# Optimization experiments

Hardware: AMD Instinct MI355X
Metric: run time of the kernel (lower is better)

The kernel has to match this reference:

```python
import jax, jax.numpy as jnp
import numpy as np

NUM_BLOCKS = 8
SPARSITY = 0.01
HARD_FRAC = 1.0
LN_EPS = 1e-5


def layer_norm(x, w, b):
    mu = jnp.mean(x, axis=-1, keepdims=True)
    var = jnp.mean(jnp.square(x - mu), axis=-1, keepdims=True)
    return (x - mu) * jax.lax.rsqrt(var + LN_EPS) * w + b


def softshrink(v, lam):
    return jnp.sign(v) * jnp.maximum(jnp.abs(v) - lam, 0.0)


def afno2d(x, w1, b1, w2, b2):
    # x: [B,H,W,C] float32
    bias = x
    B, H, W, C = x.shape
    nb = NUM_BLOCKS
    bs = C // nb
    xf = jnp.fft.rfft2(x, axes=(1, 2), norm='ortho')  # [B,H,W//2+1,C] complex
    Wf = W // 2 + 1
    xf = xf.reshape(B, H, Wf, nb, bs)
    total_modes = H // 2 + 1
    kept = int(total_modes * HARD_FRAC)
    lo = total_modes - kept
    hi = min(H, total_modes + kept)
    xs = xf[:, lo:hi, :kept]  # [B,hs,kept,nb,bs]
    xr, xi = xs.real, xs.imag
    o1r = jax.nn.relu(jnp.einsum('bhwki,kio->bhwko', xr, w1[0])
                      - jnp.einsum('bhwki,kio->bhwko', xi, w1[1]) + b1[0])
    o1i = jax.nn.relu(jnp.einsum('bhwki,kio->bhwko', xi, w1[0])
                      + jnp.einsum('bhwki,kio->bhwko', xr, w1[1]) + b1[1])
    o2r = (jnp.einsum('bhwko,koi->bhwki', o1r, w2[0])
           - jnp.einsum('bhwko,koi->bhwki', o1i, w2[1]) + b2[0])
    o2i = (jnp.einsum('bhwko,koi->bhwki', o1i, w2[0])
           + jnp.einsum('bhwko,koi->bhwki', o1r, w2[1]) + b2[1])
    o2r = softshrink(o2r, SPARSITY)
    o2i = softshrink(o2i, SPARSITY)
    oc = o2r + 1j * o2i
    full = jnp.zeros((B, H, Wf, nb, bs), dtype=oc.dtype)
    full = full.at[:, lo:hi, :kept].set(oc)
    full = full.reshape(B, H, Wf, C)
    out = jnp.fft.irfft2(full, s=(H, W), axes=(1, 2), norm='ortho')
    return out + bias


def setup_inputs() -> dict:
    key = jax.random.key(0)
    ks = jax.random.split(key, 12)
    B, H, W, C = 2, 90, 180, 768
    nb = NUM_BLOCKS
    bs = C // nb
    hidden = 4 * C
    scale = 0.02
    return {
        'x': jax.random.normal(ks[0], (B, H, W, C), jnp.float32),
        'norm1_w': jnp.ones((C,), jnp.float32),
        'norm1_b': jnp.zeros((C,), jnp.float32),
        'w1': scale * jax.random.normal(ks[1], (2, nb, bs, bs), jnp.float32),
        'b1': scale * jax.random.normal(ks[2], (2, nb, bs), jnp.float32),
        'w2': scale * jax.random.normal(ks[3], (2, nb, bs, bs), jnp.float32),
        'b2': scale * jax.random.normal(ks[4], (2, nb, bs), jnp.float32),
        'norm2_w': jnp.ones((C,), jnp.float32),
        'norm2_b': jnp.zeros((C,), jnp.float32),
        'fc1_w': jax.random.normal(ks[5], (C, hidden), jnp.float32) * (1.0 / np.sqrt(C)),
        'fc1_b': jnp.zeros((hidden,), jnp.float32),
        'fc2_w': jax.random.normal(ks[6], (hidden, C), jnp.float32) * (1.0 / np.sqrt(hidden)),
        'fc2_b': jnp.zeros((C,), jnp.float32),
    }


def reference(x, norm1_w, norm1_b, w1, b1, w2, b2, norm2_w, norm2_b,
              fc1_w, fc1_b, fc2_w, fc2_b):
    residual = x
    h = layer_norm(x, norm1_w, norm1_b)
    h = afno2d(h, w1, b1, w2, b2)
    # double_skip=True
    h = h + residual
    residual = h
    h = layer_norm(h, norm2_w, norm2_b)
    h = jax.nn.gelu(h @ fc1_w + fc1_b, approximate=False)
    h = h @ fc2_w + fc2_b
    return h + residual
```

## Files before the change

### kernel.cpp

```cpp
#include <hip/hip_runtime.h>
#include <hip/hip_bf16.h>

#define B_    2
#define H_    90
#define W_    180
#define C_    768
#define WFK   46
#define NBK   8
#define BSK   96
#define HID   3072
#define NTOK  (B_*H_*W_)
#define MPAD  32512
#define NPOS  (B_*H_*WFK)
#define LAM   0.01f

typedef __attribute__((ext_vector_type(8))) short short8;
typedef __attribute__((ext_vector_type(4))) float f32x4;

__device__ __forceinline__ float bf2f(short u) {
    union { unsigned int i; float f; } z;
    z.i = ((unsigned int)(unsigned short)u) << 16;
    return z.f;
}

__device__ __forceinline__ void gload_lds16(const void* g, void* l) {
    __builtin_amdgcn_global_load_lds((const __attribute__((address_space(1))) void*)g,
                                     (__attribute__((address_space(3))) void*)l, 16, 0, 0);
}

__device__ __forceinline__ float gelu_f(float v) {
    float u = v * (0.7978845608028654f + 0.03567740813636141f * v * v);
    float au = fabsf(u);
    float e = __expf(2.f * au);
    float t = 1.f - 2.f / (e + 1.f);
    t = copysignf(t, u);
    return 0.5f * v * (1.f + t);
}

__global__ __launch_bounds__(256) void init_tables_kernel(__hip_bfloat16* Tw, __hip_bfloat16* Twf,
                                                          __hip_bfloat16* Thf, __hip_bfloat16* Thi) {
    int i = blockIdx.x * 256 + threadIdx.x;
    const float S = 0.00785674201318386f;
    if (i < 192 * 96) {
        int w = i / 96, k = i % 96;
        int j = k >> 1, odd = k & 1;
        float val = 0.f;
        if (w < W_ && j < WFK) {
            float th = (float)((w * j) % W_) * (float)(6.283185307179586476925286766559 / 180.0);
            if (odd) val = (j == 0) ? 0.f : -2.f * S * sinf(th);
            else     val = (j == 0) ? S : 2.f * S * cosf(th);
        }
        Tw[i] = __float2bfloat16(val);
    }
    if (i < 96 * 192) {
        int r = i / 192, w = i % 192;
        int wf = r >> 1, odd = r & 1;
        float val = 0.f;
        if (w < W_ && wf < WFK) {
            float th = (float)((w * wf) % W_) * (float)(6.283185307179586476925286766559 / 180.0);
            val = odd ? -S * sinf(th) : S * cosf(th);
        }
        Twf[i] = __float2bfloat16(val);
    }
    if (i < 192 * 192) {
        int r = i / 192, j = i % 192;
        float vf = 0.f, vi = 0.f;
        if (r < 180 && j < 180) {
            int k = r >> 1, ro = r & 1, h = j >> 1, jo = j & 1;
            float th = (float)((k * h) % H_) * (float)(6.283185307179586476925286766559 / 90.0);
            float c = cosf(th), s = sinf(th);
            vf = ro ? (jo ? c : -s) : (jo ? s : c);
            vi = ro ? (jo ? c : s) : (jo ? -s : c);
        }
        Thf[i] = __float2bfloat16(vf);
        Thi[i] = __float2bfloat16(vi);
    }
}

__global__ __launch_bounds__(256) void wprep_kernel(
        const float* __restrict__ w1, const float* __restrict__ b1,
        const float* __restrict__ w2, const float* __restrict__ b2,
        __hip_bfloat16* __restrict__ wbig, float* __restrict__ bbig)
{
    int idx = blockIdx.x * 256 + threadIdx.x;
    if (idx < 2 * NBK * 192 * 192) {
        int k = idx % 192;
        int o = (idx / 192) % 192;
        int nb = (idx / (192 * 192)) % NBK;
        int L = idx / (192 * 192 * NBK);
        const float* w = L ? w2 : w1;
        const float* wr = w + (size_t)nb * BSK * BSK;
        const float* wi = w + (size_t)(NBK + nb) * BSK * BSK;
        int kk = k % BSK, oo = o % BSK;
        float val;
        if (o < BSK)  val = (k < BSK) ? wr[kk * BSK + oo] : -wi[kk * BSK + oo];
        else          val = (k < BSK) ? wi[kk * BSK + oo] :  wr[kk * BSK + oo];
        wbig[((size_t)(L * NBK + nb) * 192 + o) * 192 + k] = __float2bfloat16(val);
    }
    if (idx < 2 * NBK * 192) {
        int o = idx % 192;
        int nb = (idx / 192) % NBK;
        int L = idx / (192 * NBK);
        const float* b = L ? b2 : b1;
        bbig[idx] = (o < BSK) ? b[nb * BSK + o] : b[(NBK + nb) * BSK + (o - BSK)];
    }
}

__global__ __launch_bounds__(256) void ln_kernel(const float* __restrict__ in,
        const float* __restrict__ w, const float* __restrict__ b,
        __hip_bfloat16* __restrict__ outb, int ntok_valid)
{
    int tok = blockIdx.x;
    int tid = threadIdx.x;
    size_t base = (size_t)tok * C_;
    if (tok >= ntok_valid) {
        __hip_bfloat16 z = __float2bfloat16(0.f);
        outb[base + tid] = z; outb[base + tid + 256] = z; outb[base + tid + 512] = z;
        return;
    }
    float x0 = in[base + tid], x1 = in[base + tid + 256], x2 = in[base + tid + 512];
    float s = x0 + x1 + x2;
    float q = x0*x0 + x1*x1 + x2*x2;
#pragma unroll
    for (int off = 32; off > 0; off >>= 1) { s += __shfl_down(s, off); q += __shfl_down(q, off); }
    __shared__ float rs[4], rq[4];
    int wid = tid >> 6, lane = tid & 63;
    if (lane == 0) { rs[wid] = s; rq[wid] = q; }
    __syncthreads();
    float ts = rs[0] + rs[1] + rs[2] + rs[3];
    float tq = rq[0] + rq[1] + rq[2] + rq[3];
    float mu = ts * (1.f / C_);
    float var = tq * (1.f / C_) - mu * mu;
    float rstd = rsqrtf(var + 1e-5f);
#pragma unroll
    for (int k = 0; k < 3; ++k) {
        int c = tid + k * 256;
        float xv = (k == 0 ? x0 : (k == 1 ? x1 : x2));
        outb[base + c] = __float2bfloat16((xv - mu) * rstd * w[c] + b[c]);
    }
}

__global__ __launch_bounds__(256) void wfft_kernel(const __hip_bfloat16* __restrict__ h1,
        float* __restrict__ f1r, float* __restrict__ f1i,
        const __hip_bfloat16* __restrict__ Twf)
{
    __shared__ __hip_bfloat16 Xt[64 * 200];
    int slab = blockIdx.x;
    int c0 = blockIdx.y * 64;
    int tid = threadIdx.x, wid = tid >> 6, lane = tid & 63;
    int lrow = lane & 15, lk8 = lane >> 4;
    const short* src = (const short*)h1 + (size_t)slab * W_ * C_ + c0;
    short* X = (short*)Xt;
    for (int i = tid; i < W_ * 8; i += 256) {
        int w = i >> 3, c8 = (i & 7) * 8;
        short8 v = *(const short8*)&src[(size_t)w * C_ + c8];
#pragma unroll
        for (int j = 0; j < 8; ++j) X[(c8 + j) * 200 + w] = v[j];
    }
    for (int z = tid; z < 64 * 12; z += 256) {
        int c = z / 12, w = 180 + z % 12;
        Xt[c * 200 + w] = __float2bfloat16(0.f);
    }
    __syncthreads();
    const short* Tp = (const short*)Twf;
    f32x4 zero = {0.f, 0.f, 0.f, 0.f};
    f32x4 acc[6];
#pragma unroll
    for (int m = 0; m < 6; ++m) acc[m] = zero;
#pragma unroll
    for (int ks = 0; ks < 6; ++ks) {
        short8 bf = *(const short8*)&X[(wid * 16 + lrow) * 200 + ks * 32 + lk8 * 8];
#pragma unroll
        for (int m = 0; m < 6; ++m) {
            short8 af = *(const short8*)&Tp[(m * 16 + lrow) * 192 + ks * 32 + lk8 * 8];
            acc[m] = __builtin_amdgcn_mfma_f32_16x16x32_bf16(af, bf, acc[m], 0, 0, 0);
        }
    }
    int crow = (lane >> 4) * 4, ccol = lane & 15;
#pragma unroll
    for (int m = 0; m < 6; ++m)
#pragma unroll
        for (int j = 0; j < 4; ++j) {
            int r = m * 16 + crow + j;
            int wf = r >> 1;
            if (wf >= WFK) continue;
            size_t o = ((size_t)slab * WFK + wf) * C_ + c0 + wid * 16 + ccol;
            if (r & 1) f1i[o] = acc[m][j];
            else       f1r[o] = acc[m][j];
        }
}

__global__ __launch_bounds__(256) void hdft_kernel(float* __restrict__ dr, float* __restrict__ di,
        const __hip_bfloat16* __restrict__ Th)
{
    __shared__ __hip_bfloat16 Xt[64 * 200];
    int bwf = blockIdx.x;
    int b = bwf / WFK, wf = bwf % WFK;
    int c0 = blockIdx.y * 64;
    int tid = threadIdx.x, wid = tid >> 6, lane = tid & 63;
    int lrow = lane & 15, lk8 = lane >> 4;
    size_t base = ((size_t)(b * H_) * WFK + wf) * C_ + c0;
    short* X = (short*)Xt;
    for (int i = tid; i < H_ * 16; i += 256) {
        int h = i >> 4, cq = (i & 15) * 4;
        size_t a = base + (size_t)h * WFK * C_ + cq;
        float4 re = *(const float4*)&dr[a];
        float4 im = *(const float4*)&di[a];
        X[(cq + 0) * 200 + 2 * h]     = (short)__bfloat16_as_ushort(__float2bfloat16(re.x));
        X[(cq + 0) * 200 + 2 * h + 1] = (short)__bfloat16_as_ushort(__float2bfloat16(im.x));
        X[(cq + 1) * 200 + 2 * h]     = (short)__bfloat16_as_ushort(__float2bfloat16(re.y));
        X[(cq + 1) * 200 + 2 * h + 1] = (short)__bfloat16_as_ushort(__float2bfloat16(im.y));
        X[(cq + 2) * 200 + 2 * h]     = (short)__bfloat16_as_ushort(__float2bfloat16(re.z));
        X[(cq + 2) * 200 + 2 * h + 1] = (short)__bfloat16_as_ushort(__float2bfloat16(im.z));
        X[(cq + 3) * 200 + 2 * h]     = (short)__bfloat16_as_ushort(__float2bfloat16(re.w));
        X[(cq + 3) * 200 + 2 * h + 1] = (short)__bfloat16_as_ushort(__float2bfloat16(im.w));
    }
    for (int z = tid; z < 64 * 12; z += 256) {
        int c = z / 12, j = 180 + z % 12;
        Xt[c * 200 + j] = __float2bfloat16(0.f);
    }
    __syncthreads();
    const short* Tp = (const short*)Th;
    f32x4 zero = {0.f, 0.f, 0.f, 0.f};
    f32x4 acc[3][4];
#pragma unroll
    for (int m = 0; m < 3; ++m)
#pragma unroll
        for (int n = 0; n < 4; ++n) acc[m][n] = zero;
#pragma unroll
    for (int ks = 0; ks < 6; ++ks) {
        short8 af[3], bf[4];
#pragma unroll
        for (int m = 0; m < 3; ++m)
            af[m] = *(const short8*)&Tp[(wid * 48 + m * 16 + lrow) * 192 + ks * 32 + lk8 * 8];
#pragma unroll
        for (int n = 0; n < 4; ++n)
            bf[n] = *(const short8*)&X[(n * 16 + lrow) * 200 + ks * 32 + lk8 * 8];
#pragma unroll
        for (int m = 0; m < 3; ++m)
#pragma unroll
            for (int n = 0; n < 4; ++n)
                acc[m][n] = __builtin_amdgcn_mfma_f32_16x16x32_bf16(af[m], bf[n], acc[m][n], 0, 0, 0);
    }
    int crow = (lane >> 4) * 4, ccol = lane & 15;
#pragma unroll
    for (int m = 0; m < 3; ++m)
#pragma unroll
        for (int j = 0; j < 4; ++j) {
            int r = wid * 48 + m * 16 + crow + j;
            int kh = r >> 1;
            if (kh >= H_) continue;
#pragma unroll
            for (int n = 0; n < 4; ++n) {
                size_t o = base + (size_t)kh * WFK * C_ + n * 16 + ccol;
                if (r & 1) di[o] = acc[m][n][j];
                else       dr[o] = acc[m][n][j];
            }
        }
}

__global__ __launch_bounds__(256) void blockmlp_mfma_kernel(
        float* __restrict__ vr, float* __restrict__ vi,
        const __hip_bfloat16* __restrict__ wbig, const float* __restrict__ bbig)
{
    __shared__ __hip_bfloat16 X1[64 * 200];
    __shared__ __hip_bfloat16 X2[64 * 200];
    int chunk = blockIdx.x;
    int nb = blockIdx.y;
    int tid = threadIdx.x, wid = tid >> 6, lane = tid & 63;
    int p0 = chunk * 64;
    for (int i = tid; i < 64 * 48; i += 256) {
        int p = i / 48, q = i % 48;
        int pg = p0 + p;
        int c4 = (q % 24) * 4;
        bool isr = q < 24;
        float4 v = make_float4(0, 0, 0, 0);
        if (pg < NPOS) {
            const float* src = isr ? vr : vi;
            v = *(const float4*)&src[(size_t)pg * C_ + nb * BSK + c4];
        }
        __hip_bfloat16* d = &X1[p * 200 + (isr ? 0 : 96) + c4];
        d[0] = __float2bfloat16(v.x); d[1] = __float2bfloat16(v.y);
        d[2] = __float2bfloat16(v.z); d[3] = __float2bfloat16(v.w);
    }
    __syncthreads();
    int n0 = wid * 48;
    int lrow = lane & 15, lk8 = lane >> 4;
    int crow = (lane >> 4) * 4, ccol = lane & 15;
    const short* W1 = (const short*)(wbig + (size_t)nb * 192 * 192);
    const short* W2 = (const short*)(wbig + (size_t)(NBK + nb) * 192 * 192);
    const float* bb1 = bbig + nb * 192;
    const float* bb2 = bbig + (NBK + nb) * 192;
    f32x4 zero = {0.f, 0.f, 0.f, 0.f};
    {
        f32x4 acc[4][3];
#pragma unroll
        for (int m = 0; m < 4; ++m)
#pragma unroll
            for (int n = 0; n < 3; ++n) acc[m][n] = zero;
#pragma unroll
        for (int k0 = 0; k0 < 192; k0 += 32) {
            short8 af[4], bf[3];
#pragma unroll
            for (int m = 0; m < 4; ++m)
                af[m] = *(const short8*)&X1[(m * 16 + lrow) * 200 + k0 + lk8 * 8];
#pragma unroll
            for (int n = 0; n < 3; ++n)
                bf[n] = *(const short8*)&W1[(size_t)(n0 + n * 16 + lrow) * 192 + k0 + lk8 * 8];
#pragma unroll
            for (int m = 0; m < 4; ++m)
#pragma unroll
                for (int n = 0; n < 3; ++n)
                    acc[m][n] = __builtin_amdgcn_mfma_f32_16x16x32_bf16(af[m], bf[n], acc[m][n], 0, 0, 0);
        }
        __syncthreads();
#pragma unroll
        for (int m = 0; m < 4; ++m)
#pragma unroll
            for (int j = 0; j < 4; ++j) {
                int row = m * 16 + crow + j;
#pragma unroll
                for (int n = 0; n < 3; ++n) {
                    int col = n0 + n * 16 + ccol;
                    float v = acc[m][n][j] + bb1[col];
                    X2[row * 200 + col] = __float2bfloat16(fmaxf(v, 0.f));
                }
            }
    }
    __syncthreads();
    {
        f32x4 acc[4][3];
#pragma unroll
        for (int m = 0; m < 4; ++m)
#pragma unroll
            for (int n = 0; n < 3; ++n) acc[m][n] = zero;
#pragma unroll
        for (int k0 = 0; k0 < 192; k0 += 32) {
            short8 af[4], bf[3];
#pragma unroll
            for (int m = 0; m < 4; ++m)
                af[m] = *(const short8*)&X2[(m * 16 + lrow) * 200 + k0 + lk8 * 8];
#pragma unroll
            for (int n = 0; n < 3; ++n)
                bf[n] = *(const short8*)&W2[(size_t)(n0 + n * 16 + lrow) * 192 + k0 + lk8 * 8];
#pragma unroll
            for (int m = 0; m < 4; ++m)
#pragma unroll
                for (int n = 0; n < 3; ++n)
                    acc[m][n] = __builtin_amdgcn_mfma_f32_16x16x32_bf16(af[m], bf[n], acc[m][n], 0, 0, 0);
        }
#pragma unroll
        for (int m = 0; m < 4; ++m)
#pragma unroll
            for (int j = 0; j < 4; ++j) {
                int row = m * 16 + crow + j;
                int pg = p0 + row;
                if (pg >= NPOS) continue;
#pragma unroll
                for (int n = 0; n < 3; ++n) {
                    int col = n0 + n * 16 + ccol;
                    float v = acc[m][n][j] + bb2[col];
                    v = v > LAM ? v - LAM : (v < -LAM ? v + LAM : 0.f);
                    if (col < BSK) vr[(size_t)pg * C_ + nb * BSK + col] = v;
                    else           vi[(size_t)pg * C_ + nb * BSK + col - BSK] = v;
                }
            }
    }
}

__global__ __launch_bounds__(256) void iwfft_kernel(
        const float* __restrict__ inr, const float* __restrict__ ini,
        const __hip_bfloat16* __restrict__ h1, const float* __restrict__ x,
        float* __restrict__ out, const __hip_bfloat16* __restrict__ Tw)
{
    __shared__ __hip_bfloat16 Yt[64 * 104];
    int slab = blockIdx.x;
    int c0 = blockIdx.y * 64;
    int tid = threadIdx.x, wid = tid >> 6, lane = tid & 63;
    int lrow = lane & 15, lk8 = lane >> 4;
    size_t sb = (size_t)slab * WFK * C_ + c0;
    for (int i = tid; i < WFK * 16; i += 256) {
        int wf = i >> 4, cq = (i & 15) * 4;
        size_t a = sb + (size_t)wf * C_ + cq;
        float4 vrv = *(const float4*)&inr[a];
        float4 viv = *(const float4*)&ini[a];
        Yt[(cq + 0) * 104 + 2 * wf]     = __float2bfloat16(vrv.x);
        Yt[(cq + 0) * 104 + 2 * wf + 1] = __float2bfloat16(viv.x);
        Yt[(cq + 1) * 104 + 2 * wf]     = __float2bfloat16(vrv.y);
        Yt[(cq + 1) * 104 + 2 * wf + 1] = __float2bfloat16(viv.y);
        Yt[(cq + 2) * 104 + 2 * wf]     = __float2bfloat16(vrv.z);
        Yt[(cq + 2) * 104 + 2 * wf + 1] = __float2bfloat16(viv.z);
        Yt[(cq + 3) * 104 + 2 * wf]     = __float2bfloat16(vrv.w);
        Yt[(cq + 3) * 104 + 2 * wf + 1] = __float2bfloat16(viv.w);
    }
    {
        int c = tid >> 2, kk = 92 + (tid & 3);
        Yt[c * 104 + kk] = __float2bfloat16(0.f);
    }
    __syncthreads();
    const short* Tp = (const short*)Tw;
    f32x4 zero = {0.f, 0.f, 0.f, 0.f};
    f32x4 acc[3][4];
#pragma unroll
    for (int m = 0; m < 3; ++m)
#pragma unroll
        for (int n = 0; n < 4; ++n) acc[m][n] = zero;
#pragma unroll
    for (int ks = 0; ks < 3; ++ks) {
        short8 af[3], bf[4];
#pragma unroll
        for (int m = 0; m < 3; ++m)
            af[m] = *(const short8*)&Tp[(wid * 48 + m * 16 + lrow) * 96 + ks * 32 + lk8 * 8];
#pragma unroll
        for (int n = 0; n < 4; ++n)
            bf[n] = *(const short8*)&Yt[(n * 16 + lrow) * 104 + ks * 32 + lk8 * 8];
#pragma unroll
        for (int m = 0; m < 3; ++m)
#pragma unroll
            for (int n = 0; n < 4; ++n)
                acc[m][n] = __builtin_amdgcn_mfma_f32_16x16x32_bf16(af[m], bf[n], acc[m][n], 0, 0, 0);
    }
    int crow = (lane >> 4) * 4, ccol = lane & 15;
    const short* hp = (const short*)h1;
#pragma unroll
    for (int m = 0; m < 3; ++m)
#pragma unroll
        for (int j = 0; j < 4; ++j) {
            int w = wid * 48 + m * 16 + crow + j;
            if (w >= W_) continue;
            size_t o = ((size_t)slab * W_ + w) * C_ + c0;
#pragma unroll
            for (int n = 0; n < 4; ++n) {
                int col = n * 16 + ccol;
                out[o + col] = acc[m][n][j] + bf2f(hp[o + col]) + x[o + col];
            }
        }
}

__global__ __launch_bounds__(256) void transpose_cvt_kernel(const float* __restrict__ Wm,
        __hip_bfloat16* __restrict__ Wt, int R, int Ccol)
{
    __shared__ float tile[32][33];
    int c0 = blockIdx.x * 32, r0 = blockIdx.y * 32;
    int tid = threadIdx.x;
    int tc = tid & 31, tr = tid >> 5;
#pragma unroll
    for (int k = 0; k < 4; ++k)
        tile[tr + k * 8][tc] = Wm[(size_t)(r0 + tr + k * 8) * Ccol + c0 + tc];
    __syncthreads();
    int rr = tid & 31, cc = tid >> 5;
#pragma unroll
    for (int k = 0; k < 4; ++k)
        Wt[(size_t)(c0 + cc + k * 8) * R + r0 + rr] = __float2bfloat16(tile[rr][cc + k * 8]);
}

template<int EPI>
__global__ __launch_bounds__(512, 1) void gemm_kernel(
        const short* __restrict__ A, const short* __restrict__ Bt,
        const float* __restrict__ bias,
        __hip_bfloat16* __restrict__ obf, float* __restrict__ of32,
        const float* __restrict__ res, int N, int K, int mvalid, int MT, int NT)
{
    __shared__ short lds[49152];
    int nwg = MT * NT;
    int orig = blockIdx.x;
    int xcd = orig & 7, loc = orig >> 3;
    int q = nwg >> 3, rm = nwg & 7;
    int wg = (xcd < rm ? xcd * (q + 1) : rm * (q + 1) + (xcd - rm) * q) + loc;
    const int SUPER = 4;
    int per = SUPER * NT;
    int sidx = wg / per, offs = wg % per;
    int rows = MT - sidx * SUPER; if (rows > SUPER) rows = SUPER;
    int mt = sidx * SUPER + offs % rows;
    int nt = offs / rows;
    size_t m0 = (size_t)mt * 256, n0 = (size_t)nt * 128;

    int tid = threadIdx.x;
    int wid = tid >> 6, lane = tid & 63;
    int wmidx = wid >> 1, wnidx = wid & 1;
    int lrow = lane & 15, lk8 = lane >> 4;
    int rswz = (lk8 ^ ((lrow >> 1) & 3)) * 16;

    int sr = tid >> 2;
    int soct = (tid & 3) ^ ((sr >> 1) & 3);
    const short* Agbase = A + (m0 + sr) * (size_t)K + soct * 8;
    const short* Bgbase = Bt + (n0 + sr) * (size_t)K + soct * 8;
    int dA = sr * 64 + (tid & 3) * 16;
    f32x4 zero = {0.f, 0.f, 0.f, 0.f};
    f32x4 acc[4][4];
#pragma unroll
    for (int i = 0; i < 4; ++i)
#pragma unroll
        for (int j = 0; j < 4; ++j) acc[i][j] = zero;

    auto stagepair = [&](int buf, int kt, int ksh) {
        const short* As = Agbase + kt * 64 + ksh * 32;
        char* Ad = (char*)lds + buf * 32768 + ksh * 16384 + dA;
        gload_lds16(As, Ad);
        gload_lds16(As + (size_t)128 * K, Ad + 8192);
        const short* Bs = Bgbase + kt * 64 + ksh * 32;
        char* Bd = (char*)lds + 65536 + buf * 16384 + ksh * 8192 + dA;
        gload_lds16(Bs, Bd);
    };

    int abase = (wmidx * 64 + lrow) * 64 + rswz;
    int bbase = 65536 + (wnidx * 64 + lrow) * 64 + rswz;
    auto phase = [&](int buf, int ks, int kt_stage, bool do_stage, int waitN) {
        const char* L = (const char*)lds;
        short8 af[4], bfr[4];
        int ao = buf * 32768 + ks * 16384 + abase;
        int bo = buf * 16384 + ks * 8192 + bbase;
#pragma unroll
        for (int mf = 0; mf < 4; ++mf) af[mf] = *(const short8*)(L + ao + mf * 1024);
#pragma unroll
        for (int nf = 0; nf < 4; ++nf) bfr[nf] = *(const short8*)(L + bo + nf * 1024);
        if (do_stage) stagepair(buf ^ 1, kt_stage, ks);
        __builtin_amdgcn_sched_barrier(0);
        __builtin_amdgcn_s_barrier();
        asm volatile("s_waitcnt lgkmcnt(0)" ::: "memory");
        __builtin_amdgcn_sched_barrier(0);
        __builtin_amdgcn_s_setprio(1);
#pragma unroll
        for (int mf = 0; mf < 4; ++mf)
#pragma unroll
            for (int nf = 0; nf < 4; ++nf)
                acc[mf][nf] = __builtin_amdgcn_mfma_f32_16x16x32_bf16(af[mf], bfr[nf], acc[mf][nf], 0, 0, 0);
        __builtin_amdgcn_s_setprio(0);
        if (waitN == 0)      asm volatile("s_waitcnt vmcnt(0)" ::: "memory");
        else if (waitN > 0)  asm volatile("s_waitcnt vmcnt(3)" ::: "memory");
        __builtin_amdgcn_sched_barrier(0);
        __builtin_amdgcn_s_barrier();
        __builtin_amdgcn_sched_barrier(0);
    };

    int NK = K >> 6;
    stagepair(0, 0, 0);
    stagepair(0, 0, 1);
    asm volatile("s_waitcnt vmcnt(3)" ::: "memory");
    __builtin_amdgcn_sched_barrier(0);
    __builtin_amdgcn_s_barrier();
    for (int t = 0; t < NK; ++t) {
        int buf = t & 1;
        bool last = (t == NK - 1);
        phase(buf, 0, t + 1, !last, last ? 0 : 1);
        phase(buf, 1, t + 1, !last, last ? -1 : 1);
    }

    int crow = (lane >> 4) * 4;
    int ccol = lane & 15;
#pragma unroll
    for (int mf = 0; mf < 4; ++mf) {
#pragma unroll
        for (int j = 0; j < 4; ++j) {
            size_t r = m0 + wmidx * 64 + mf * 16 + crow + j;
            if (EPI == 1 && r >= (size_t)mvalid) continue;
#pragma unroll
            for (int nf = 0; nf < 4; ++nf) {
                size_t cidx = n0 + wnidx * 64 + nf * 16 + ccol;
                float v = acc[mf][nf][j] + bias[cidx];
                if (EPI == 0) {
                    obf[r * N + cidx] = __float2bfloat16(gelu_f(v));
                } else {
                    of32[r * N + cidx] = v + res[r * N + cidx];
                }
            }
        }
    }
}

extern "C" void kernel_launch(void* const* d_in, const int* in_sizes, int n_in,
                              void* d_out, int out_size, void* d_ws, size_t ws_size,
                              hipStream_t stream) {
    (void)in_sizes; (void)n_in; (void)out_size;
    const float* x    = (const float*)d_in[0];
    const float* n1w  = (const float*)d_in[1];
    const float* n1b  = (const float*)d_in[2];
    const float* w1   = (const float*)d_in[3];
    const float* b1   = (const float*)d_in[4];
    const float* w2   = (const float*)d_in[5];
    const float* b2   = (const float*)d_in[6];
    const float* n2w  = (const float*)d_in[7];
    const float* n2b  = (const float*)d_in[8];
    const float* fc1w = (const float*)d_in[9];
    const float* fc1b = (const float*)d_in[10];
    const float* fc2w = (const float*)d_in[11];
    const float* fc2b = (const float*)d_in[12];
    float* out = (float*)d_out;

    const size_t fl_region1 = (size_t)MPAD * C_ / 2;
    const size_t fl_f1      = (size_t)2 * NPOS * C_;
    const size_t fl_tb1     = (size_t)MPAD * HID / 2;
    const size_t fl_tb2     = (size_t)64 * 256 * HID / 2;
    const size_t fl_wx      = 2712576 + 4096;
    const size_t need1 = (fl_region1 + fl_tb1 + fl_wx) * 4;
    const size_t need2 = (fl_region1 + ((fl_f1 > fl_tb2) ? fl_f1 : fl_tb2) + fl_wx) * 4;
    int nch = (ws_size >= need1) ? 1 : (ws_size >= need2) ? 2 : 4;
    size_t fl_tb = (nch == 1) ? fl_tb1 : (nch == 2) ? fl_tb2 : 0;
    size_t fl_big = (fl_f1 > fl_tb) ? fl_f1 : fl_tb;

    float* wsf = (float*)d_ws;
    size_t off = 0;
    auto alloc = [&](size_t nfloats) { float* p = wsf + off; off += (nfloats + 63) & ~(size_t)63; return p; };
    float* region1   = alloc(fl_region1);
    float* regionBig = alloc(fl_big);
    __hip_bfloat16* w1t = (__hip_bfloat16*)alloc((size_t)HID * C_ / 2);
    __hip_bfloat16* w2t = (__hip_bfloat16*)alloc((size_t)HID * C_ / 2);
    __hip_bfloat16* wbig = (__hip_bfloat16*)alloc((size_t)2 * NBK * 192 * 192 / 2);
    float* bbig = alloc(2 * NBK * 192);
    __hip_bfloat16* Tw  = (__hip_bfloat16*)alloc(192 * 96 / 2);
    __hip_bfloat16* Twf = (__hip_bfloat16*)alloc(96 * 192 / 2);
    __hip_bfloat16* Thf = (__hip_bfloat16*)alloc(192 * 192 / 2);
    __hip_bfloat16* Thi = (__hip_bfloat16*)alloc(192 * 192 / 2);

    __hip_bfloat16* h1b = (__hip_bfloat16*)region1;
    __hip_bfloat16* h3  = (__hip_bfloat16*)region1;
    float* f1r = regionBig;
    float* f1i = regionBig + (size_t)NPOS * C_;
    __hip_bfloat16* tb  = (__hip_bfloat16*)regionBig;

    init_tables_kernel<<<144, 256, 0, stream>>>(Tw, Twf, Thf, Thi);
    wprep_kernel<<<(2 * NBK * 192 * 192 + 255) / 256, 256, 0, stream>>>(w1, b1, w2, b2, wbig, bbig);
    transpose_cvt_kernel<<<dim3(HID / 32, C_ / 32), 256, 0, stream>>>(fc1w, w1t, C_, HID);
    transpose_cvt_kernel<<<dim3(C_ / 32, HID / 32), 256, 0, stream>>>(fc2w, w2t, HID, C_);

    ln_kernel<<<NTOK, 256, 0, stream>>>(x, n1w, n1b, h1b, NTOK);
    wfft_kernel<<<dim3(B_ * H_, 12), 256, 0, stream>>>(h1b, f1r, f1i, Twf);
    hdft_kernel<<<dim3(B_ * WFK, 12), 256, 0, stream>>>(f1r, f1i, Thf);
    blockmlp_mfma_kernel<<<dim3(130, NBK), 256, 0, stream>>>(f1r, f1i, wbig, bbig);
    hdft_kernel<<<dim3(B_ * WFK, 12), 256, 0, stream>>>(f1r, f1i, Thi);
    iwfft_kernel<<<dim3(B_ * H_, 12), 256, 0, stream>>>(f1r, f1i, h1b, x, out, Tw);
    ln_kernel<<<MPAD, 256, 0, stream>>>(out, n2w, n2b, h3, NTOK);

    int tilesArr[4], ntiles = 0;
    if (nch == 1)      { tilesArr[0] = 127; ntiles = 1; }
    else if (nch == 2) { tilesArr[0] = 64; tilesArr[1] = 63; ntiles = 2; }
    else               { tilesArr[0] = 32; tilesArr[1] = 32; tilesArr[2] = 32; tilesArr[3] = 31; ntiles = 4; }
    int baseT = 0;
    for (int c = 0; c < ntiles; ++c) {
        int tiles = tilesArr[c];
        size_t baseRow = (size_t)baseT * 256;
        gemm_kernel<0><<<tiles * (HID / 128), 512, 0, stream>>>(
            (const short*)(h3 + baseRow * C_), (const short*)w1t, fc1b,
            tb, nullptr, nullptr, HID, C_, 0, tiles, HID / 128);
        gemm_kernel<1><<<tiles * (C_ / 128), 512, 0, stream>>>(
            (const short*)tb, (const short*)w2t, fc2b,
            nullptr, out + baseRow * C_, out + baseRow * C_, C_, HID, NTOK - (int)baseRow, tiles, C_ / 128);
        baseT += tiles;
    }
}
```

Measured before the change: 761.4 us.

## Store spectral intermediates as bf16 and triple-buffer GEMM LDS staging

The frequency-domain intermediates between the W-FFT, H-DFT, block MLP and inverse transforms are now stored in bf16 instead of fp32. This halves their global memory traffic and lets the loaders use 16-byte short8 loads with no conversion. Separately, the dense MLP GEMM moves from a two-buffer, per-half-K staging scheme to a three-deep LDS ring, prefetching two K-tiles ahead with one barrier per tile. This raises LDS use to 144 KB per block, which may limit occupancy, and the extra bf16 rounding of intermediates adds some precision loss.

```diff
diff --git a/kernel.cpp b/kernel.cpp
--- a/kernel.cpp
+++ b/kernel.cpp
@@ -21,6 +21,9 @@
     union { unsigned int i; float f; } z;
     z.i = ((unsigned int)(unsigned short)u) << 16;
     return z.f;
+}
+__device__ __forceinline__ short f2b(float f) {
+    return (short)__bfloat16_as_ushort(__float2bfloat16(f));
 }
 
 __device__ __forceinline__ void gload_lds16(const void* g, void* l) {
@@ -141,7 +144,7 @@
 }
 
 __global__ __launch_bounds__(256) void wfft_kernel(const __hip_bfloat16* __restrict__ h1,
-        float* __restrict__ f1r, float* __restrict__ f1i,
+        short* __restrict__ f1r, short* __restrict__ f1i,
         const __hip_bfloat16* __restrict__ Twf)
 {
     __shared__ __hip_bfloat16 Xt[64 * 200];
@@ -185,12 +188,12 @@
             int wf = r >> 1;
             if (wf >= WFK) continue;
             size_t o = ((size_t)slab * WFK + wf) * C_ + c0 + wid * 16 + ccol;
-            if (r & 1) f1i[o] = acc[m][j];
-            else       f1r[o] = acc[m][j];
-        }
-}
-
-__global__ __launch_bounds__(256) void hdft_kernel(float* __restrict__ dr, float* __restrict__ di,
+            if (r & 1) f1i[o] = f2b(acc[m][j]);
+            else       f1r[o] = f2b(acc[m][j]);
+        }
+}
+
+__global__ __launch_bounds__(256) void hdft_kernel(short* __restrict__ dr, short* __restrict__ di,
         const __hip_bfloat16* __restrict__ Th)
 {
     __shared__ __hip_bfloat16 Xt[64 * 200];
@@ -201,19 +204,16 @@
     int lrow = lane & 15, lk8 = lane >> 4;
     size_t base = ((size_t)(b * H_) * WFK + wf) * C_ + c0;
     short* X = (short*)Xt;
-    for (int i = tid; i < H_ * 16; i += 256) {
-        int h = i >> 4, cq = (i & 15) * 4;
-        size_t a = base + (size_t)h * WFK * C_ + cq;
-        float4 re = *(const float4*)&dr[a];
-        float4 im = *(const float4*)&di[a];
-        X[(cq + 0) * 200 + 2 * h]     = (short)__bfloat16_as_ushort(__float2bfloat16(re.x));
-        X[(cq + 0) * 200 + 2 * h + 1] = (short)__bfloat16_as_ushort(__float2bfloat16(im.x));
-        X[(cq + 1) * 200 + 2 * h]     = (short)__bfloat16_as_ushort(__float2bfloat16(re.y));
-        X[(cq + 1) * 200 + 2 * h + 1] = (short)__bfloat16_as_ushort(__float2bfloat16(im.y));
-        X[(cq + 2) * 200 + 2 * h]     = (short)__bfloat16_as_ushort(__float2bfloat16(re.z));
-        X[(cq + 2) * 200 + 2 * h + 1] = (short)__bfloat16_as_ushort(__float2bfloat16(im.z));
-        X[(cq + 3) * 200 + 2 * h]     = (short)__bfloat16_as_ushort(__float2bfloat16(re.w));
-        X[(cq + 3) * 200 + 2 * h + 1] = (short)__bfloat16_as_ushort(__float2bfloat16(im.w));
+    for (int i = tid; i < H_ * 8; i += 256) {
+        int h = i >> 3, c8 = (i & 7) * 8;
+        size_t a = base + (size_t)h * WFK * C_ + c8;
+        short8 re = *(const short8*)&dr[a];
+        short8 im = *(const short8*)&di[a];
+#pragma unroll
+        for (int j = 0; j < 8; ++j) {
+            X[(c8 + j) * 200 + 2 * h]     = re[j];
+            X[(c8 + j) * 200 + 2 * h + 1] = im[j];
+        }
     }
     for (int z = tid; z < 64 * 12; z += 256) {
         int c = z / 12, j = 180 + z % 12;
@@ -253,14 +253,14 @@
 #pragma unroll
             for (int n = 0; n < 4; ++n) {
                 size_t o = base + (size_t)kh * WFK * C_ + n * 16 + ccol;
-                if (r & 1) di[o] = acc[m][n][j];
-                else       dr[o] = acc[m][n][j];
+                if (r & 1) di[o] = f2b(acc[m][n][j]);
+                else       dr[o] = f2b(acc[m][n][j]);
             }
         }
 }
 
 __global__ __launch_bounds__(256) void blockmlp_mfma_kernel(
-        float* __restrict__ vr, float* __restrict__ vi,
+        short* __restrict__ vr, short* __restrict__ vi,
         const __hip_bfloat16* __restrict__ wbig, const float* __restrict__ bbig)
 {
     __shared__ __hip_bfloat16 X1[64 * 200];
@@ -269,19 +269,20 @@
     int nb = blockIdx.y;
     int tid = threadIdx.x, wid = tid >> 6, lane = tid & 63;
     int p0 = chunk * 64;
-    for (int i = tid; i < 64 * 48; i += 256) {
-        int p = i / 48, q = i % 48;
+    short8 z8 = {0, 0, 0, 0, 0, 0, 0, 0};
+    for (int i = tid; i < 64 * 24; i += 256) {
+        int p = i / 24, q = i % 24;
         int pg = p0 + p;
-        int c4 = (q % 24) * 4;
-        bool isr = q < 24;
-        float4 v = make_float4(0, 0, 0, 0);
+        bool isr = q < 12;
+        int c8 = (q % 12) * 8;
+        short8 v = z8;
         if (pg < NPOS) {
-            const float* src = isr ? vr : vi;
-            v = *(const float4*)&src[(size_t)pg * C_ + nb * BSK + c4];
-        }
-        __hip_bfloat16* d = &X1[p * 200 + (isr ? 0 : 96) + c4];
-        d[0] = __float2bfloat16(v.x); d[1] = __float2bfloat16(v.y);
-        d[2] = __float2bfloat16(v.z); d[3] = __float2bfloat16(v.w);
+            const short* src = isr ? vr : vi;
+            v = *(const short8*)&src[(size_t)pg * C_ + nb * BSK + c8];
+        }
+        short* d = (short*)&X1[p * 200 + (isr ? 0 : 96) + c8];
+#pragma unroll
+        for (int j = 0; j < 8; ++j) d[j] = v[j];
     }
     __syncthreads();
     int n0 = wid * 48;
@@ -361,15 +362,15 @@
                     int col = n0 + n * 16 + ccol;
                     float v = acc[m][n][j] + bb2[col];
                     v = v > LAM ? v - LAM : (v < -LAM ? v + LAM : 0.f);
-                    if (col < BSK) vr[(size_t)pg * C_ + nb * BSK + col] = v;
-                    else           vi[(size_t)pg * C_ + nb * BSK + col - BSK] = v;
+                    if (col < BSK) vr[(size_t)pg * C_ + nb * BSK + col] = f2b(v);
+                    else           vi[(size_t)pg * C_ + nb * BSK + col - BSK] = f2b(v);
                 }
             }
     }
 }
 
 __global__ __launch_bounds__(256) void iwfft_kernel(
-        const float* __restrict__ inr, const float* __restrict__ ini,
+        const short* __restrict__ inr, const short* __restrict__ ini,
         const __hip_bfloat16* __restrict__ h1, const float* __restrict__ x,
         float* __restrict__ out, const __hip_bfloat16* __restrict__ Tw)
 {
@@ -379,19 +380,17 @@
     int tid = threadIdx.x, wid = tid >> 6, lane = tid & 63;
     int lrow = lane & 15, lk8 = lane >> 4;
     size_t sb = (size_t)slab * WFK * C_ + c0;
-    for (int i = tid; i < WFK * 16; i += 256) {
-        int wf = i >> 4, cq = (i & 15) * 4;
-        size_t a = sb + (size_t)wf * C_ + cq;
-        float4 vrv = *(const float4*)&inr[a];
-        float4 viv = *(const float4*)&ini[a];
-        Yt[(cq + 0) * 104 + 2 * wf]     = __float2bfloat16(vrv.x);
-        Yt[(cq + 0) * 104 + 2 * wf + 1] = __float2bfloat16(viv.x);
-        Yt[(cq + 1) * 104 + 2 * wf]     = __float2bfloat16(vrv.y);
-        Yt[(cq + 1) * 104 + 2 * wf + 1] = __float2bfloat16(viv.y);
-        Yt[(cq + 2) * 104 + 2 * wf]     = __float2bfloat16(vrv.z);
-        Yt[(cq + 2) * 104 + 2 * wf + 1] = __float2bfloat16(viv.z);
-        Yt[(cq + 3) * 104 + 2 * wf]     = __float2bfloat16(vrv.w);
-        Yt[(cq + 3) * 104 + 2 * wf + 1] = __float2bfloat16(viv.w);
+    short* Y = (short*)Yt;
+    for (int i = tid; i < WFK * 8; i += 256) {
+        int wf = i >> 3, c8 = (i & 7) * 8;
+        size_t a = sb + (size_t)wf * C_ + c8;
+        short8 re = *(const short8*)&inr[a];
+        short8 im = *(const short8*)&ini[a];
+#pragma unroll
+        for (int j = 0; j < 8; ++j) {
+            Y[(c8 + j) * 104 + 2 * wf]     = re[j];
+            Y[(c8 + j) * 104 + 2 * wf + 1] = im[j];
+        }
     }
     {
         int c = tid >> 2, kk = 92 + (tid & 3);
@@ -413,7 +412,7 @@
             af[m] = *(const short8*)&Tp[(wid * 48 + m * 16 + lrow) * 96 + ks * 32 + lk8 * 8];
 #pragma unroll
         for (int n = 0; n < 4; ++n)
-            bf[n] = *(const short8*)&Yt[(n * 16 + lrow) * 104 + ks * 32 + lk8 * 8];
+            bf[n] = *(const short8*)&Y[(n * 16 + lrow) * 104 + ks * 32 + lk8 * 8];
 #pragma unroll
         for (int m = 0; m < 3; ++m)
 #pragma unroll
@@ -461,7 +460,7 @@
         __hip_bfloat16* __restrict__ obf, float* __restrict__ of32,
         const float* __restrict__ res, int N, int K, int mvalid, int MT, int NT)
 {
-    __shared__ short lds[49152];
+    __shared__ short lds[73728];
     int nwg = MT * NT;
     int orig = blockIdx.x;
     int xcd = orig & 7, loc = orig >> 3;
@@ -493,57 +492,56 @@
 #pragma unroll
         for (int j = 0; j < 4; ++j) acc[i][j] = zero;
 
-    auto stagepair = [&](int buf, int kt, int ksh) {
-        const short* As = Agbase + kt * 64 + ksh * 32;
-        char* Ad = (char*)lds + buf * 32768 + ksh * 16384 + dA;
-        gload_lds16(As, Ad);
-        gload_lds16(As + (size_t)128 * K, Ad + 8192);
-        const short* Bs = Bgbase + kt * 64 + ksh * 32;
-        char* Bd = (char*)lds + 65536 + buf * 16384 + ksh * 8192 + dA;
-        gload_lds16(Bs, Bd);
+    auto stage = [&](int buf, int kt) {
+        const short* As0 = Agbase + kt * 64;
+        const short* Bs0 = Bgbase + kt * 64;
+        char* Ab = (char*)lds + buf * 49152 + dA;
+        char* Bb = (char*)lds + buf * 49152 + 32768 + dA;
+#pragma unroll
+        for (int ksh = 0; ksh < 2; ++ksh) {
+            gload_lds16(As0 + ksh * 32, Ab + ksh * 16384);
+            gload_lds16(As0 + ksh * 32 + (size_t)128 * K, Ab + ksh * 16384 + 8192);
+            gload_lds16(Bs0 + ksh * 32, Bb + ksh * 8192);
+        }
     };
 
     int abase = (wmidx * 64 + lrow) * 64 + rswz;
-    int bbase = 65536 + (wnidx * 64 + lrow) * 64 + rswz;
-    auto phase = [&](int buf, int ks, int kt_stage, bool do_stage, int waitN) {
-        const char* L = (const char*)lds;
-        short8 af[4], bfr[4];
-        int ao = buf * 32768 + ks * 16384 + abase;
-        int bo = buf * 16384 + ks * 8192 + bbase;
-#pragma unroll
-        for (int mf = 0; mf < 4; ++mf) af[mf] = *(const short8*)(L + ao + mf * 1024);
-#pragma unroll
-        for (int nf = 0; nf < 4; ++nf) bfr[nf] = *(const short8*)(L + bo + nf * 1024);
-        if (do_stage) stagepair(buf ^ 1, kt_stage, ks);
-        __builtin_amdgcn_sched_barrier(0);
-        __builtin_amdgcn_s_barrier();
-        asm volatile("s_waitcnt lgkmcnt(0)" ::: "memory");
-        __builtin_amdgcn_sched_barrier(0);
-        __builtin_amdgcn_s_setprio(1);
-#pragma unroll
-        for (int mf = 0; mf < 4; ++mf)
-#pragma unroll
-            for (int nf = 0; nf < 4; ++nf)
-                acc[mf][nf] = __builtin_amdgcn_mfma_f32_16x16x32_bf16(af[mf], bfr[nf], acc[mf][nf], 0, 0, 0);
-        __builtin_amdgcn_s_setprio(0);
-        if (waitN == 0)      asm volatile("s_waitcnt vmcnt(0)" ::: "memory");
-        else if (waitN > 0)  asm volatile("s_waitcnt vmcnt(3)" ::: "memory");
+    int bbase = 32768 + (wnidx * 64 + lrow) * 64 + rswz;
+
+    int NK = K >> 6;
+    stage(0, 0); stage(1, 1);
+    for (int t = 0; t < NK; ++t) {
+        int buf = t % 3;
+        if (t + 2 < NK) stage((t + 2) % 3, t + 2);
+        if (t + 2 < NK)      asm volatile("s_waitcnt vmcnt(12)" ::: "memory");
+        else if (t + 1 < NK) asm volatile("s_waitcnt vmcnt(6)" ::: "memory");
+        else                 asm volatile("s_waitcnt vmcnt(0)" ::: "memory");
         __builtin_amdgcn_sched_barrier(0);
         __builtin_amdgcn_s_barrier();
         __builtin_amdgcn_sched_barrier(0);
-    };
-
-    int NK = K >> 6;
-    stagepair(0, 0, 0);
-    stagepair(0, 0, 1);
-    asm volatile("s_waitcnt vmcnt(3)" ::: "memory");
-    __builtin_amdgcn_sched_barrier(0);
-    __builtin_amdgcn_s_barrier();
-    for (int t = 0; t < NK; ++t) {
-        int buf = t & 1;
-        bool last = (t == NK - 1);
-        phase(buf, 0, t + 1, !last, last ? 0 : 1);
-        phase(buf, 1, t + 1, !last, last ? -1 : 1);
+#pragma unroll
+        for (int ks = 0; ks < 2; ++ks) {
+            const char* L = (const char*)lds;
+            short8 af[4], bfr[4];
+            int ao = buf * 49152 + ks * 16384 + abase;
+            int bo = buf * 49152 + ks * 8192 + bbase;
+#pragma unroll
+            for (int mf = 0; mf < 4; ++mf) af[mf] = *(const short8*)(L + ao + mf * 1024);
+#pragma unroll
+            for (int nf = 0; nf < 4; ++nf) bfr[nf] = *(const short8*)(L + bo + nf * 1024);
+            asm volatile("s_waitcnt lgkmcnt(0)" ::: "memory");
+            __builtin_amdgcn_sched_barrier(0);
+            __builtin_amdgcn_s_setprio(1);
+#pragma unroll
+            for (int mf = 0; mf < 4; ++mf)
+#pragma unroll
+                for (int nf = 0; nf < 4; ++nf)
+                    acc[mf][nf] = __builtin_amdgcn_mfma_f32_16x16x32_bf16(af[mf], bfr[nf], acc[mf][nf], 0, 0, 0);
+            __builtin_amdgcn_s_setprio(0);
+        }
+        __builtin_amdgcn_sched_barrier(0);
+        __builtin_amdgcn_s_barrier();
+        __builtin_amdgcn_sched_barrier(0);
     }
 
     int crow = (lane >> 4) * 4;
@@ -588,7 +586,7 @@
     float* out = (float*)d_out;
 
     const size_t fl_region1 = (size_t)MPAD * C_ / 2;
-    const size_t fl_f1      = (size_t)2 * NPOS * C_;
+    const size_t fl_f1      = (size_t)NPOS * C_;
     const size_t fl_tb1     = (size_t)MPAD * HID / 2;
     const size_t fl_tb2     = (size_t)64 * 256 * HID / 2;
     const size_t fl_wx      = 2712576 + 4096;
@@ -614,8 +612,8 @@
 
     __hip_bfloat16* h1b = (__hip_bfloat16*)region1;
     __hip_bfloat16* h3  = (__hip_bfloat16*)region1;
-    float* f1r = regionBig;
-    float* f1i = regionBig + (size_t)NPOS * C_;
+    short* f1r = (short*)regionBig;
+    short* f1i = f1r + (size_t)NPOS * C_;
     __hip_bfloat16* tb  = (__hip_bfloat16*)regionBig;
 
     init_tables_kernel<<<144, 256, 0, stream>>>(Tw, Twf, Thf, Thi);
```

Result: slower. 802.0 us (+5.3%).
